# Performance work log

Measured on AMD Instinct MI355X. Metric: run time of the kernel, lower is better.

Reference implementation:

```python
import jax, jax.numpy as jnp
import numpy as np

WINDOW = 3
FILTER = 6
FEATURE = 768
SEQ = 256
PAD = WINDOW // 2


def setup_inputs() -> dict:
    key = jax.random.key(0)
    k1, k2, k3 = jax.random.split(key, 3)
    B = 256
    inputs = jax.random.normal(k1, (B, SEQ, FEATURE), dtype=jnp.float32)
    # per-position Linear weights: torch nn.Linear stores [out, in]; we keep [S, in, out]
    bound = 1.0 / np.sqrt(WINDOW * FEATURE)
    W = jax.random.uniform(k2, (SEQ, WINDOW * FEATURE, FILTER), dtype=jnp.float32,
                           minval=-bound, maxval=bound)
    b = jax.random.uniform(k3, (SEQ, FILTER), dtype=jnp.float32,
                           minval=-bound, maxval=bound)
    return {"inputs": inputs, "W": W, "b": b}


def reference(inputs, W, b):
    # inputs: [B, S, F]. Pad along sequence with zeros (matches F.pad on transposed tensor).
    padded = jnp.pad(inputs, ((0, 0), (PAD, PAD), (0, 0)))  # [B, S+2p, F]
    # Vectorized sliding-window gather: idx [S, W]
    idx = jnp.arange(SEQ)[:, None] + jnp.arange(WINDOW)[None, :]
    windows = padded[:, idx, :]                              # [B, S, W, F]
    Bsz = windows.shape[0]
    windows = windows.reshape(Bsz, SEQ, WINDOW * FEATURE)    # [B, S, W*F]
    # Per-position distinct Linear + ReLU (Dropout is identity at inference)
    out = jnp.einsum('bsf,sfo->bso', windows, W) + b[None, :, :]
    return jax.nn.relu(out)
```

## Files before the change

### kernel.cpp

```cpp
#include <hip/hip_runtime.h>

#define SEQ    256
#define FEAT   768
#define WIN    3
#define FILT   6
#define KTOT   (WIN * FEAT)
#define WELEMS (KTOT * FILT)
#define NB     8
#define BLOCK  1024
#define NWAVES (BLOCK / 64)
#define BATCH  256
#define NGROUPS (BATCH / NB)

__global__ __launch_bounds__(BLOCK, 4)
void pos_linear_kernel(const float* __restrict__ x,
                       const float* __restrict__ W,
                       const float* __restrict__ bias,
                       float* __restrict__ out) {
    __shared__ float wlds[WELEMS];
    const int s   = blockIdx.x;
    const int tid = threadIdx.x;

    {
        const float4* src = (const float4*)(W + (size_t)s * WELEMS);
        float4*       dst = (float4*)wlds;
        for (int i = tid; i < WELEMS / 4; i += BLOCK) dst[i] = src[i];
    }
    __syncthreads();

    const int lane = tid & 63;
    const int wave = tid >> 6;

    for (int g = wave; g < NGROUPS; g += NWAVES) {
        const int b0 = g * NB;

        float acc[NB][FILT];
        #pragma unroll
        for (int nb = 0; nb < NB; ++nb)
            #pragma unroll
            for (int o = 0; o < FILT; ++o) acc[nb][o] = 0.f;

        #pragma unroll
        for (int w = 0; w < WIN; ++w) {
            const int r = s - 1 + w;
            if (r < 0 || r >= SEQ) continue;
            const float* xrow0 = x + ((size_t)b0 * SEQ + r) * FEAT;
            const float* wbase = wlds + w * FEAT * FILT;

            for (int i = 0; i < FEAT / 64; ++i) {
                const int f = lane + 64 * i;

                float wv[FILT];
                #pragma unroll
                for (int o = 0; o < FILT; ++o) wv[o] = wbase[f * FILT + o];

                float xv[NB];
                #pragma unroll
                for (int nb = 0; nb < NB; ++nb)
                    xv[nb] = xrow0[(size_t)nb * SEQ * FEAT + f];

                #pragma unroll
                for (int nb = 0; nb < NB; ++nb)
                    #pragma unroll
                    for (int o = 0; o < FILT; ++o)
                        acc[nb][o] = fmaf(xv[nb], wv[o], acc[nb][o]);
            }
        }

        float vals[NB * FILT];
        #pragma unroll
        for (int nb = 0; nb < NB; ++nb)
            #pragma unroll
            for (int o = 0; o < FILT; ++o) vals[nb * FILT + o] = acc[nb][o];

        #pragma unroll
        for (int m = 1; m < 64; m <<= 1) {
            #pragma unroll
            for (int i = 0; i < NB * FILT; ++i)
                vals[i] += __shfl_xor(vals[i], m, 64);
        }

        if (lane < NB * FILT) {
            float v = vals[0];
            #pragma unroll
            for (int i = 1; i < NB * FILT; ++i) v = (lane == i) ? vals[i] : v;
            const int nb = lane / FILT;
            const int o  = lane - nb * FILT;
            v += bias[s * FILT + o];
            v = v > 0.f ? v : 0.f;
            out[((size_t)(b0 + nb) * SEQ + s) * FILT + o] = v;
        }
    }
}

extern "C" void kernel_launch(void* const* d_in, const int* in_sizes, int n_in,
                              void* d_out, int out_size, void* d_ws, size_t ws_size,
                              hipStream_t stream) {
    const float* x  = (const float*)d_in[0];
    const float* W  = (const float*)d_in[1];
    const float* b  = (const float*)d_in[2];
    float*       out = (float*)d_out;
    (void)in_sizes; (void)n_in; (void)out_size; (void)d_ws; (void)ws_size;
    pos_linear_kernel<<<SEQ, BLOCK, 0, stream>>>(x, W, b, out);
}
```

Baseline: 341.8 us.

## Vectorize x loads to float4, pad LDS weight chunks, use halving-tree reduction

Each lane now processes four consecutive features per iteration, loading x as float4 and reading its 24 weights as six float4 LDS loads. The weights are stored in padded chunks with a stride of 7 float4s to avoid LDS bank conflicts. The 48-value cross-lane reduction is replaced by a recursive-halving exchange, which cuts the number of shuffles from 48 per step to progressively fewer. The risks are higher register pressure from 24 weights plus 8 float4 x values, and more complex output index mapping.

```diff
diff --git a/kernel.cpp b/kernel.cpp
--- a/kernel.cpp
+++ b/kernel.cpp
@@ -6,6 +6,8 @@
 #define FILT   6
 #define KTOT   (WIN * FEAT)
 #define WELEMS (KTOT * FILT)
+#define NCHUNK (WELEMS / 24)
+#define CSTR4  7
 #define NB     8
 #define BLOCK  1024
 #define NWAVES (BLOCK / 64)
@@ -17,14 +19,16 @@
                        const float* __restrict__ W,
                        const float* __restrict__ bias,
                        float* __restrict__ out) {
-    __shared__ float wlds[WELEMS];
+    __shared__ float4 wlds4[NCHUNK * CSTR4];
     const int s   = blockIdx.x;
     const int tid = threadIdx.x;
 
     {
         const float4* src = (const float4*)(W + (size_t)s * WELEMS);
-        float4*       dst = (float4*)wlds;
-        for (int i = tid; i < WELEMS / 4; i += BLOCK) dst[i] = src[i];
+        for (int i = tid; i < WELEMS / 4; i += BLOCK) {
+            const int c = i / 6, j = i - c * 6;
+            wlds4[c * CSTR4 + j] = src[i];
+        }
     }
     __syncthreads();
 
@@ -45,50 +49,71 @@
             const int r = s - 1 + w;
             if (r < 0 || r >= SEQ) continue;
             const float* xrow0 = x + ((size_t)b0 * SEQ + r) * FEAT;
-            const float* wbase = wlds + w * FEAT * FILT;
 
-            for (int i = 0; i < FEAT / 64; ++i) {
-                const int f = lane + 64 * i;
+            for (int i = 0; i < FEAT / 256; ++i) {
+                const int f4 = lane + 64 * i;
 
-                float wv[FILT];
-                #pragma unroll
-                for (int o = 0; o < FILT; ++o) wv[o] = wbase[f * FILT + o];
+                float4 wv4[6];
+                {
+                    const float4* wc = wlds4 + (size_t)(w * (FEAT / 4) + f4) * CSTR4;
+                    #pragma unroll
+                    for (int rr = 0; rr < 6; ++rr) wv4[rr] = wc[rr];
+                }
+                const float* wv = (const float*)wv4;
 
-                float xv[NB];
+                float4 xv[NB];
                 #pragma unroll
                 for (int nb = 0; nb < NB; ++nb)
-                    xv[nb] = xrow0[(size_t)nb * SEQ * FEAT + f];
+                    xv[nb] = *(const float4*)(xrow0 + (size_t)nb * SEQ * FEAT + 4 * f4);
 
                 #pragma unroll
-                for (int nb = 0; nb < NB; ++nb)
+                for (int nb = 0; nb < NB; ++nb) {
+                    const float* xf = (const float*)&xv[nb];
                     #pragma unroll
-                    for (int o = 0; o < FILT; ++o)
-                        acc[nb][o] = fmaf(xv[nb], wv[o], acc[nb][o]);
+                    for (int ff = 0; ff < 4; ++ff)
+                        #pragma unroll
+                        for (int o = 0; o < FILT; ++o)
+                            acc[nb][o] = fmaf(xf[ff], wv[ff * FILT + o], acc[nb][o]);
+                }
             }
         }
 
-        float vals[NB * FILT];
+        float v[NB * FILT];
         #pragma unroll
         for (int nb = 0; nb < NB; ++nb)
             #pragma unroll
-            for (int o = 0; o < FILT; ++o) vals[nb * FILT + o] = acc[nb][o];
+            for (int o = 0; o < FILT; ++o) v[nb * FILT + o] = acc[nb][o];
 
         #pragma unroll
-        for (int m = 1; m < 64; m <<= 1) {
+        for (int step = 0; step < 4; ++step) {
+            const int m = 1 << step;
+            const int half = 48 >> (step + 1);
+            const bool upper = (lane & m) != 0;
             #pragma unroll
-            for (int i = 0; i < NB * FILT; ++i)
-                vals[i] += __shfl_xor(vals[i], m, 64);
+            for (int j = 0; j < half; ++j) {
+                float snd = upper ? v[j] : v[j + half];
+                float kep = upper ? v[j + half] : v[j];
+                v[j] = kep + __shfl_xor(snd, m, 64);
+            }
+        }
+        #pragma unroll
+        for (int j = 0; j < 3; ++j) {
+            v[j] += __shfl_xor(v[j], 16, 64);
+            v[j] += __shfl_xor(v[j], 32, 64);
         }
 
-        if (lane < NB * FILT) {
-            float v = vals[0];
+        if (lane < 16) {
+            const int gidx = ((lane & 1) << 3) | ((lane & 2) << 1) |
+                             ((lane & 4) >> 1) | ((lane & 8) >> 3);
             #pragma unroll
-            for (int i = 1; i < NB * FILT; ++i) v = (lane == i) ? vals[i] : v;
-            const int nb = lane / FILT;
-            const int o  = lane - nb * FILT;
-            v += bias[s * FILT + o];
-            v = v > 0.f ? v : 0.f;
-            out[((size_t)(b0 + nb) * SEQ + s) * FILT + o] = v;
+            for (int j = 0; j < 3; ++j) {
+                const int idx = 3 * gidx + j;
+                const int nb  = idx / FILT;
+                const int o   = idx - nb * FILT;
+                float r0 = v[j] + bias[s * FILT + o];
+                r0 = r0 > 0.f ? r0 : 0.f;
+                out[((size_t)(b0 + nb) * SEQ + s) * FILT + o] = r0;
+            }
         }
     }
 }
@@ -96,9 +121,9 @@
 extern "C" void kernel_launch(void* const* d_in, const int* in_sizes, int n_in,
                               void* d_out, int out_size, void* d_ws, size_t ws_size,
                               hipStream_t stream) {
-    const float* x  = (const float*)d_in[0];
-    const float* W  = (const float*)d_in[1];
-    const float* b  = (const float*)d_in[2];
+    const float* x   = (const float*)d_in[0];
+    const float* W   = (const float*)d_in[1];
+    const float* b   = (const float*)d_in[2];
     float*       out = (float*)d_out;
     (void)in_sizes; (void)n_in; (void)out_size; (void)d_ws; (void)ws_size;
     pos_linear_kernel<<<SEQ, BLOCK, 0, stream>>>(x, W, b, out);
```

Result: no change. 348.0 us (+1.8%).
